# Kernel tuning notes

Hardware: AMD Instinct MI355X
Metric: run time of the kernel (lower is better)

The kernel has to match this reference:

```python
import jax, jax.numpy as jnp
import numpy as np

# Model constants (match init_kwargs / input_specs)
D_MODEL = 64; N_HEADS = 4; D_HEAD = D_MODEL // N_HEADS
N_LAYERS = 2; D_FF = 256
N_GRAPHS = 256; NODES_PER = 64; N_NODES = N_GRAPHS * NODES_PER
DEG = 8; N_EDGES = N_NODES * DEG
VOCAB = 32; N_CLASS = 10


def setup_inputs() -> dict:
    rng = np.random.default_rng(0)
    # node labels
    x = jnp.asarray(rng.integers(0, VOCAB, N_NODES), dtype=jnp.int32)
    # sparse edge_index: each node receives DEG messages from random nodes in its own graph
    base = np.repeat(np.arange(N_NODES), DEG)
    nbr = (base // NODES_PER) * NODES_PER + rng.integers(0, NODES_PER, N_NODES * DEG)
    edge_index = jnp.asarray(np.stack([nbr, base]), dtype=jnp.int32)  # [2, E] (src, dst)
    # complete_edge_index: all (src, dst) pairs within each graph
    local = np.arange(NODES_PER); goff = np.arange(N_GRAPHS) * NODES_PER
    ii = np.repeat(local, NODES_PER); jj = np.tile(local, NODES_PER)
    c_src = (goff[:, None] + ii[None, :]).reshape(-1)
    c_dst = (goff[:, None] + jj[None, :]).reshape(-1)
    complete_edge_index = jnp.asarray(np.stack([c_src, c_dst]), dtype=jnp.int32)  # [2, 1048576]
    batch = jnp.asarray(np.repeat(np.arange(N_GRAPHS), NODES_PER), dtype=jnp.int32)

    key = jax.random.key(0)
    ks = jax.random.split(key, 12)
    s = 1.0 / np.sqrt(D_MODEL)
    W = lambda k, shape, sc: jax.random.normal(k, shape, jnp.float32) * sc
    return {
        'x': x, 'edge_index': edge_index, 'complete_edge_index': complete_edge_index, 'batch': batch,
        'emb': W(ks[0], (VOCAB, D_MODEL), 0.1),
        'Wg_self': W(ks[1], (N_LAYERS, D_MODEL, D_MODEL), s),
        'Wg_nbr': W(ks[2], (N_LAYERS, D_MODEL, D_MODEL), s),
        'Wq': W(ks[3], (N_LAYERS, D_MODEL, D_MODEL), s),
        'Wk': W(ks[4], (N_LAYERS, D_MODEL, D_MODEL), s),
        'Wv': W(ks[5], (N_LAYERS, D_MODEL, D_MODEL), s),
        'Wo': W(ks[6], (N_LAYERS, D_MODEL, D_MODEL), s),
        'bo': jnp.zeros((N_LAYERS, D_MODEL), jnp.float32),
        'ln1_g': jnp.ones((N_LAYERS, D_MODEL), jnp.float32),
        'ln1_b': jnp.zeros((N_LAYERS, D_MODEL), jnp.float32),
        'ff_W1': W(ks[7], (N_LAYERS, D_MODEL, D_FF), s),
        'ff_b1': jnp.zeros((N_LAYERS, D_FF), jnp.float32),
        'ff_W2': W(ks[8], (N_LAYERS, D_FF, D_MODEL), 1.0 / np.sqrt(D_FF)),
        'ff_b2': jnp.zeros((N_LAYERS, D_MODEL), jnp.float32),
        'ln2_g': jnp.ones((N_LAYERS, D_MODEL), jnp.float32),
        'ln2_b': jnp.zeros((N_LAYERS, D_MODEL), jnp.float32),
        'c_W1': W(ks[9], (D_MODEL, D_MODEL), s),
        'c_b1': jnp.zeros((D_MODEL,), jnp.float32),
        'c_W2': W(ks[10], (D_MODEL, N_CLASS), s),
        'c_b2': jnp.zeros((N_CLASS,), jnp.float32),
    }


def _layernorm(h, g, b):
    m = jnp.mean(h, -1, keepdims=True)
    v = jnp.var(h, -1, keepdims=True)
    return (h - m) * jax.lax.rsqrt(v + 1e-5) * g + b


def _forward(x, edge_index, complete_edge_index, batch, emb, Wg_self, Wg_nbr, Wq, Wk, Wv, Wo, bo,
             ln1_g, ln1_b, ff_W1, ff_b1, ff_W2, ff_b2, ln2_g, ln2_b, c_W1, c_b1, c_W2, c_b2):
    e_src, e_dst = edge_index[0], edge_index[1]
    c_src, c_dst = complete_edge_index[0], complete_edge_index[1]
    h = emb[x]  # [N, d] embedding lookup
    inv_sqrt = 1.0 / np.sqrt(D_HEAD)
    for i in range(N_LAYERS):
        # --- structure extractor: one GNN message-passing step over sparse edge_index ---
        agg = jax.ops.segment_sum((h @ Wg_nbr[i])[e_src], e_dst, num_segments=N_NODES)
        struct = h + jax.nn.relu(h @ Wg_self[i] + agg)
        # --- multi-head attention over complete_edge_index (full attention within graph) ---
        q = (struct @ Wq[i]).reshape(N_NODES, N_HEADS, D_HEAD)
        k = (struct @ Wk[i]).reshape(N_NODES, N_HEADS, D_HEAD)
        v = (h @ Wv[i]).reshape(N_NODES, N_HEADS, D_HEAD)
        scores = jnp.einsum('ehd,ehd->eh', q[c_dst], k[c_src]) * inv_sqrt  # [Ec, H]
        m = jax.ops.segment_max(scores, c_dst, num_segments=N_NODES)
        ex = jnp.exp(scores - m[c_dst])
        den = jax.ops.segment_sum(ex, c_dst, num_segments=N_NODES)
        alpha = ex / den[c_dst]  # segment softmax per destination node
        attn = jax.ops.segment_sum(alpha[:, :, None] * v[c_src], c_dst, num_segments=N_NODES)
        out = attn.reshape(N_NODES, D_MODEL) @ Wo[i] + bo[i]
        h = _layernorm(h + out, ln1_g[i], ln1_b[i])
        # --- feed-forward ---
        f = jax.nn.relu(h @ ff_W1[i] + ff_b1[i]) @ ff_W2[i] + ff_b2[i]
        h = _layernorm(h + f, ln2_g[i], ln2_b[i])
    # --- global mean pooling per graph + classifier ---
    counts = jax.ops.segment_sum(jnp.ones((N_NODES,), jnp.float32), batch, num_segments=N_GRAPHS)
    pooled = jax.ops.segment_sum(h, batch, num_segments=N_GRAPHS) / counts[:, None]
    return jax.nn.relu(pooled @ c_W1 + c_b1) @ c_W2 + c_b2  # [B, num_class]


def reference(x, edge_index, complete_edge_index, batch, emb, Wg_self, Wg_nbr, Wq, Wk, Wv, Wo, bo,
              ln1_g, ln1_b, ff_W1, ff_b1, ff_W2, ff_b2, ln2_g, ln2_b, c_W1, c_b1, c_W2, c_b2):
    return _forward(x, edge_index, complete_edge_index, batch, emb, Wg_self, Wg_nbr, Wq, Wk, Wv, Wo,
                    bo, ln1_g, ln1_b, ff_W1, ff_b1, ff_W2, ff_b2, ln2_g, ln2_b, c_W1, c_b1, c_W2, c_b2)
```

## Files before the change

### kernel.cpp

```cpp
#include <hip/hip_runtime.h>

#define NG 256
#define NPG 64
#define DM 64
#define DFF 256
#define NL 2
#define DEG 8
#define NCLS 10
#define S68 68
#define S132 132

#define HB0 0
#define AB0 4352
#define BB0 8704
#define QB0 13056
#define F10 17408
#define POOLW 25856

#define FF1B 98304
#define FF2B 163840
#define WTOT 229376

__device__ __align__(16) unsigned short g_w[WTOT];

typedef __attribute__((ext_vector_type(4))) float f32x4;
typedef __attribute__((ext_vector_type(4))) unsigned int u32x4;
typedef __attribute__((ext_vector_type(8))) __bf16 bf16x8;

__device__ __forceinline__ unsigned int packsplit(float x) {
    union { float f; unsigned int u; } a; a.f = x;
    const unsigned int t = a.u;
    const unsigned int hi = (t + 0x7FFFu + ((t >> 16) & 1u)) >> 16;
    union { unsigned int u; float f; } hf; hf.u = hi << 16;
    union { float f; unsigned int u; } b; b.f = x - hf.f;
    const unsigned int tl = b.u;
    const unsigned int lo = (tl + 0x7FFFu + ((tl >> 16) & 1u)) & 0xFFFF0000u;
    return hi | lo;
}
__device__ __forceinline__ float unpackf(unsigned int u) {
    union { unsigned int u; float f; } h, l;
    h.u = u << 16;
    l.u = u & 0xFFFF0000u;
    return h.f + l.f;
}

__device__ __forceinline__ void extract(u32x4 p0, u32x4 p1, u32x4& hi, u32x4& lo) {
    hi[0] = (p0[0] & 0xFFFFu) | (p0[1] << 16);
    hi[1] = (p0[2] & 0xFFFFu) | (p0[3] << 16);
    hi[2] = (p1[0] & 0xFFFFu) | (p1[1] << 16);
    hi[3] = (p1[2] & 0xFFFFu) | (p1[3] << 16);
    lo[0] = (p0[0] >> 16) | (p0[1] & 0xFFFF0000u);
    lo[1] = (p0[2] >> 16) | (p0[3] & 0xFFFF0000u);
    lo[2] = (p1[0] >> 16) | (p1[1] & 0xFFFF0000u);
    lo[3] = (p1[2] >> 16) | (p1[3] & 0xFFFF0000u);
}

__device__ __forceinline__ bf16x8 ld8(const unsigned short* p) { return *(const bf16x8*)p; }

__device__ __forceinline__ f32x4 mfma16(u32x4 a, bf16x8 b, f32x4 c) {
    return __builtin_amdgcn_mfma_f32_16x16x32_bf16(__builtin_bit_cast(bf16x8, a), b, c, 0, 0, 0);
}

struct AP2 { u32x4 h, l; };
__device__ __forceinline__ AP2 loadA32(const unsigned int* p) {
    const u32x4 a0 = *(const u32x4*)p, a1 = *(const u32x4*)(p + 4);
    AP2 r; extract(a0, a1, r.h, r.l); return r;
}

__device__ __forceinline__ f32x4 chunkp(const AP2& a, const unsigned short* bhp, int plane,
                                        f32x4 acc) {
    const bf16x8 bh = ld8(bhp), bl = ld8(bhp + plane);
    acc = mfma16(a.h, bh, acc);
    acc = mfma16(a.h, bl, acc);
    acc = mfma16(a.l, bh, acc);
    return acc;
}

__device__ __forceinline__ f32x4 mm64p(const AP2& a0, const AP2& a1,
                                       const unsigned short* Wh, int boff) {
    f32x4 acc = {0.f, 0.f, 0.f, 0.f};
    acc = chunkp(a0, Wh + boff,      4096, acc);
    acc = chunkp(a1, Wh + boff + 32, 4096, acc);
    return acc;
}

__device__ __forceinline__ void dwrite_f32(float* dst, f32x4 acc, int wr, int wc, int l) {
    const int col = (wc << 4) + (l & 15);
    const int r0 = (wr << 4) + ((l >> 4) << 2);
#pragma unroll
    for (int r = 0; r < 4; ++r) dst[(r0 + r) * S68 + col] = acc[r];
}

__device__ __forceinline__ void layernorm(const float* src, unsigned int* dst,
                                          const float* gp, const float* bp, int n, int jg) {
    const f32x4 v = *(const f32x4*)(src + n * S68 + jg);
    float s1 = v[0] + v[1] + v[2] + v[3];
    float s2 = v[0]*v[0] + v[1]*v[1] + v[2]*v[2] + v[3]*v[3];
    s1 += __shfl_xor(s1, 1); s1 += __shfl_xor(s1, 2);
    s1 += __shfl_xor(s1, 4); s1 += __shfl_xor(s1, 8);
    s2 += __shfl_xor(s2, 1); s2 += __shfl_xor(s2, 2);
    s2 += __shfl_xor(s2, 4); s2 += __shfl_xor(s2, 8);
    const float mean = s1 * 0.015625f;
    const float var  = s2 * 0.015625f - mean * mean;
    const float rstd = rsqrtf(var + 1e-5f);
    const f32x4 gm = *(const f32x4*)(gp + jg);
    const f32x4 bt = *(const f32x4*)(bp + jg);
    u32x4 p;
#pragma unroll
    for (int j = 0; j < 4; ++j) p[j] = packsplit((v[j] - mean) * rstd * gm[j] + bt[j]);
    *(u32x4*)(dst + n * S68 + jg) = p;
}

extern "C" __global__ void gt_prep(const float* __restrict__ Wgn, const float* __restrict__ Wgs,
                                   const float* __restrict__ Wk, const float* __restrict__ Wq,
                                   const float* __restrict__ Wv, const float* __restrict__ Wo,
                                   const float* __restrict__ fW1, const float* __restrict__ fW2,
                                   unsigned short* wout)
{
    unsigned short* W = wout ? wout : g_w;
    const int t = blockIdx.x * 256 + threadIdx.x;
    float v; int dhi, plane;
    if (t < 49152) {
        const int m = t >> 12, r = t & 4095, k = r >> 6, c = r & 63;
        const int lay = m / 6, idx = m - lay * 6;
        const float* s;
        switch (idx) { case 0: s = Wgn; break; case 1: s = Wgs; break;
                       case 2: s = Wk;  break; case 3: s = Wq;  break;
                       case 4: s = Wv;  break; default: s = Wo; }
        v = s[lay * 4096 + k * 64 + c];
        dhi = (m << 13) + (c << 6) + k;
        plane = 4096;
    } else if (t < 81920) {
        const int r = t - 49152, lay = r >> 14, q = r & 16383, k = q >> 8, c = q & 255;
        v = fW1[lay * 16384 + k * 256 + c];
        dhi = FF1B + lay * 32768 + (c << 6) + k;
        plane = 16384;
    } else {
        const int r = t - 81920, lay = r >> 14, q = r & 16383, k = q >> 6, c = q & 63;
        v = fW2[lay * 16384 + k * 64 + c];
        dhi = FF2B + lay * 32768 + (c << 8) + k;
        plane = 16384;
    }
    union { float f; unsigned int u; } a; a.f = v;
    const unsigned int hi = (a.u + 0x7FFFu + ((a.u >> 16) & 1u)) >> 16;
    union { unsigned int u; float f; } hf; hf.u = hi << 16;
    union { float f; unsigned int u; } b; b.f = v - hf.f;
    const unsigned int lo = (b.u + 0x7FFFu + ((b.u >> 16) & 1u)) >> 16;
    W[dhi] = (unsigned short)hi;
    W[dhi + plane] = (unsigned short)lo;
}

extern "C" __global__ __launch_bounds__(1024)
void gt_main(const int* __restrict__ x, const int* __restrict__ e_src,
             const float* __restrict__ emb, const float* __restrict__ bo,
             const float* __restrict__ l1g, const float* __restrict__ l1b,
             const float* __restrict__ fb1, const float* __restrict__ fb2,
             const float* __restrict__ l2g, const float* __restrict__ l2b,
             const float* __restrict__ cW1, const float* __restrict__ cb1,
             const float* __restrict__ cW2, const float* __restrict__ cb2,
             const unsigned short* __restrict__ wext,
             float* __restrict__ out)
{
    const unsigned short* gww = wext ? wext : g_w;

    __shared__ __align__(16) unsigned int pool[POOLW];
    unsigned int* Hb  = pool + HB0;
    unsigned int* Abu = pool + AB0;  float* Abf = (float*)Abu;
    float* Bbf = (float*)(pool + BB0);
    float* Qbf = (float*)(pool + QB0);
    float* Vbf = (float*)(pool + F10);
    unsigned int* F1  = pool + F10;

    const int g = blockIdx.x, tid = threadIdx.x;
    const int w = tid >> 6, l = tid & 63;
    const int wr = w >> 2, wc = w & 3;
    const int n = tid >> 4, jg = (tid & 15) << 2;

    const int arow = (wr << 4) + (l & 15);
    const int bcol = (wc << 4) + (l & 15);
    const int kg   = (l >> 4) << 3;
    const int boff = (bcol << 6) + kg;

    {
        const int lbl = x[g * NPG + n];
        const f32x4 e = *(const f32x4*)(emb + lbl * DM + jg);
        u32x4 p;
#pragma unroll
        for (int j = 0; j < 4; ++j) p[j] = packsplit(e[j]);
        *(u32x4*)(Hb + n * S68 + jg) = p;
    }
    __syncthreads();

    for (int lay = 0; lay < NL; ++lay) {
        const unsigned short* Wm = gww + ((lay * 6) << 13);

        {
            const unsigned int* Ar = Hb + arow * S68;
            const AP2 a0 = loadA32(Ar + kg), a1 = loadA32(Ar + kg + 32);
            dwrite_f32(Abf, mm64p(a0, a1, Wm,               boff), wr, wc, l);
            dwrite_f32(Qbf, mm64p(a0, a1, Wm + (1 << 13),   boff), wr, wc, l);
            dwrite_f32(Vbf, mm64p(a0, a1, Wm + (4 << 13),   boff), wr, wc, l);
        }
        __syncthreads();

        {
            f32x4 s = {0.f, 0.f, 0.f, 0.f};
            const int* es = e_src + (g * NPG + n) * DEG;
#pragma unroll
            for (int k = 0; k < DEG; ++k) {
                const int sr = es[k] - g * NPG;
                const f32x4 v4 = *(const f32x4*)(Abf + sr * S68 + jg);
                s[0] += v4[0]; s[1] += v4[1]; s[2] += v4[2]; s[3] += v4[3];
            }
            *(f32x4*)(Bbf + n * S68 + jg) = s;
        }
        __syncthreads();

        {
            const f32x4 u4 = *(const f32x4*)(Qbf + n * S68 + jg);
            const f32x4 a4 = *(const f32x4*)(Bbf + n * S68 + jg);
            const u32x4 hp = *(const u32x4*)(Hb + n * S68 + jg);
            u32x4 p;
#pragma unroll
            for (int j = 0; j < 4; ++j)
                p[j] = packsplit(unpackf(hp[j]) + fmaxf(u4[j] + a4[j], 0.f));
            *(u32x4*)(Abu + n * S68 + jg) = p;
        }
        __syncthreads();

        {
            const unsigned int* Ar = Abu + arow * S68;
            const AP2 a0 = loadA32(Ar + kg), a1 = loadA32(Ar + kg + 32);
            dwrite_f32(Bbf, mm64p(a0, a1, Wm + (2 << 13), boff), wr, wc, l);
            dwrite_f32(Qbf, mm64p(a0, a1, Wm + (3 << 13), boff), wr, wc, l);
        }
        __syncthreads();

        {
            const f32x4 qr = *(const f32x4*)(Qbf + n * S68 + jg);
            const float q0 = qr[0] * 0.25f, q1 = qr[1] * 0.25f;
            const float q2 = qr[2] * 0.25f, q3 = qr[3] * 0.25f;
            float o0 = 0.f, o1 = 0.f, o2 = 0.f, o3 = 0.f, m = -1e30f, ls = 0.f;
#pragma unroll 4
            for (int sr = 0; sr < NPG; ++sr) {
                const f32x4 k4 = *(const f32x4*)(Bbf + sr * S68 + jg);
                float s = q0*k4[0] + q1*k4[1] + q2*k4[2] + q3*k4[3];
                s += __shfl_xor(s, 1);
                s += __shfl_xor(s, 2);
                const float mn  = fmaxf(m, s);
                const float fac = __expf(m - mn), wg = __expf(s - mn);
                ls = ls * fac + wg;
                const f32x4 v4 = *(const f32x4*)(Vbf + sr * S68 + jg);
                o0 = o0 * fac + wg * v4[0]; o1 = o1 * fac + wg * v4[1];
                o2 = o2 * fac + wg * v4[2]; o3 = o3 * fac + wg * v4[3];
                m = mn;
            }
            const float il = 1.f / ls;
            u32x4 p;
            p[0] = packsplit(o0 * il); p[1] = packsplit(o1 * il);
            p[2] = packsplit(o2 * il); p[3] = packsplit(o3 * il);
            *(u32x4*)(Abu + n * S68 + jg) = p;
        }
        __syncthreads();

        {
            const unsigned int* Ar = Abu + arow * S68;
            const AP2 a0 = loadA32(Ar + kg), a1 = loadA32(Ar + kg + 32);
            const f32x4 acc = mm64p(a0, a1, Wm + (5 << 13), boff);
            const int r0 = (wr << 4) + ((l >> 4) << 2);
            const float bb = bo[lay * DM + bcol];
#pragma unroll
            for (int r = 0; r < 4; ++r) {
                const int row = r0 + r;
                Bbf[row * S68 + bcol] = acc[r] + bb + unpackf(Hb[row * S68 + bcol]);
            }
        }
        __syncthreads();

        layernorm(Bbf, Hb, l1g + lay * DM, l1b + lay * DM, n, jg);
        __syncthreads();

        f32x4 f2 = {0.f, 0.f, 0.f, 0.f};
        for (int hf = 0; hf < 2; ++hf) {
            {
                const unsigned int* Ar = Hb + arow * S68;
                const AP2 a0 = loadA32(Ar + kg), a1 = loadA32(Ar + kg + 32);
                const unsigned short* B1 = gww + FF1B + lay * 32768;
                const int r0 = (wr << 4) + ((l >> 4) << 2);
#pragma unroll
                for (int t = 0; t < 2; ++t) {
                    const int tc = ((wc + 4 * t) << 4) + (l & 15);
                    const int cg = hf * 128 + tc;
                    f32x4 acc = {0.f, 0.f, 0.f, 0.f};
                    acc = chunkp(a0, B1 + (cg << 6) + kg,      16384, acc);
                    acc = chunkp(a1, B1 + (cg << 6) + kg + 32, 16384, acc);
                    const float b1 = fb1[lay * DFF + cg];
#pragma unroll
                    for (int r = 0; r < 4; ++r)
                        F1[(r0 + r) * S132 + tc] = packsplit(fmaxf(acc[r] + b1, 0.f));
                }
            }
            __syncthreads();
            {
                const unsigned int* Ar = F1 + arow * S132;
                const unsigned short* B2 = gww + FF2B + lay * 32768 + (bcol << 8) + hf * 128;
#pragma unroll
                for (int ch = 0; ch < 4; ++ch) {
                    const AP2 ac = loadA32(Ar + kg + 32 * ch);
                    f2 = chunkp(ac, B2 + kg + 32 * ch, 16384, f2);
                }
            }
            __syncthreads();
        }
        {
            const int r0 = (wr << 4) + ((l >> 4) << 2);
            const float bb = fb2[lay * DM + bcol];
#pragma unroll
            for (int r = 0; r < 4; ++r) {
                const int row = r0 + r;
                Abf[row * S68 + bcol] = f2[r] + bb + unpackf(Hb[row * S68 + bcol]);
            }
        }
        __syncthreads();

        layernorm(Abf, Hb, l2g + lay * DM, l2b + lay * DM, n, jg);
        __syncthreads();
    }

    if (tid < DM) {
        float s = 0.f;
        for (int nn = 0; nn < NPG; ++nn) s += unpackf(Hb[nn * S68 + tid]);
        Abf[tid] = s * 0.015625f;
    }
    __syncthreads();
    if (tid < DM) {
        float acc = cb1[tid];
        for (int i = 0; i < DM; ++i) acc = fmaf(Abf[i], cW1[i * DM + tid], acc);
        Bbf[tid] = fmaxf(acc, 0.f);
    }
    __syncthreads();
    if (tid < NCLS) {
        float acc = cb2[tid];
        for (int i = 0; i < DM; ++i) acc = fmaf(Bbf[i], cW2[i * NCLS + tid], acc);
        out[g * NCLS + tid] = acc;
    }
}

extern "C" void kernel_launch(void* const* d_in, const int* in_sizes, int n_in,
                              void* d_out, int out_size, void* d_ws, size_t ws_size,
                              hipStream_t stream) {
    unsigned short* wbuf =
        (d_ws != nullptr && ws_size >= (size_t)WTOT * 2) ? (unsigned short*)d_ws : nullptr;
    gt_prep<<<dim3(448), dim3(256), 0, stream>>>(
        (const float*)d_in[6], (const float*)d_in[5],
        (const float*)d_in[8], (const float*)d_in[7],
        (const float*)d_in[9], (const float*)d_in[10],
        (const float*)d_in[14], (const float*)d_in[16],
        wbuf);
    gt_main<<<dim3(NG), dim3(1024), 0, stream>>>(
        (const int*)d_in[0], (const int*)d_in[1],
        (const float*)d_in[4], (const float*)d_in[11],
        (const float*)d_in[12], (const float*)d_in[13],
        (const float*)d_in[15], (const float*)d_in[17],
        (const float*)d_in[18], (const float*)d_in[19],
        (const float*)d_in[20], (const float*)d_in[21],
        (const float*)d_in[22], (const float*)d_in[23],
        wbuf,
        (float*)d_out);
}
```

Baseline: 96.26 us.

## Stage 64x64 weights in swizzled LDS with prefetch overlapping compute phases

Weights are now stored as interleaved hi/lo bf16 pairs in one 32-bit word rather than two separate planes. The six 64x64 projection matrices per layer are staged into three XOR-swizzled LDS buffers. Each buffer is refilled from global memory during an earlier phase so the load overlaps other work, and the MFMA B operands are then read from LDS instead of global memory. This raises LDS use to about 150KB per block, which still fits at one block per CU. It also adds register pressure from prefetched values held across phases, plus extract work on the B operands.

```diff
diff --git a/kernel.cpp b/kernel.cpp
--- a/kernel.cpp
+++ b/kernel.cpp
@@ -15,13 +15,14 @@
 #define BB0 8704
 #define QB0 13056
 #define F10 17408
-#define POOLW 25856
-
-#define FF1B 98304
-#define FF2B 163840
-#define WTOT 229376
-
-__device__ __align__(16) unsigned short g_w[WTOT];
+#define WSB 25856
+#define POOLW 38144
+
+#define FF1B 49152
+#define FF2B 81920
+#define WTOT 114688
+
+__device__ __align__(16) unsigned int g_w[WTOT];
 
 typedef __attribute__((ext_vector_type(4))) float f32x4;
 typedef __attribute__((ext_vector_type(4))) unsigned int u32x4;
@@ -55,10 +56,9 @@
     lo[3] = (p1[2] >> 16) | (p1[3] & 0xFFFF0000u);
 }
 
-__device__ __forceinline__ bf16x8 ld8(const unsigned short* p) { return *(const bf16x8*)p; }
-
-__device__ __forceinline__ f32x4 mfma16(u32x4 a, bf16x8 b, f32x4 c) {
-    return __builtin_amdgcn_mfma_f32_16x16x32_bf16(__builtin_bit_cast(bf16x8, a), b, c, 0, 0, 0);
+__device__ __forceinline__ f32x4 mfma16(u32x4 a, u32x4 b, f32x4 c) {
+    return __builtin_amdgcn_mfma_f32_16x16x32_bf16(
+        __builtin_bit_cast(bf16x8, a), __builtin_bit_cast(bf16x8, b), c, 0, 0, 0);
 }
 
 struct AP2 { u32x4 h, l; };
@@ -67,20 +67,28 @@
     AP2 r; extract(a0, a1, r.h, r.l); return r;
 }
 
-__device__ __forceinline__ f32x4 chunkp(const AP2& a, const unsigned short* bhp, int plane,
-                                        f32x4 acc) {
-    const bf16x8 bh = ld8(bhp), bl = ld8(bhp + plane);
+__device__ __forceinline__ f32x4 chunkAB(const AP2& a, u32x4 w0, u32x4 w1, f32x4 acc) {
+    u32x4 bh, bl;
+    extract(w0, w1, bh, bl);
     acc = mfma16(a.h, bh, acc);
     acc = mfma16(a.h, bl, acc);
     acc = mfma16(a.l, bh, acc);
     return acc;
 }
-
-__device__ __forceinline__ f32x4 mm64p(const AP2& a0, const AP2& a1,
-                                       const unsigned short* Wh, int boff) {
+__device__ __forceinline__ f32x4 chunkG(const AP2& a, const unsigned int* p, f32x4 acc) {
+    return chunkAB(a, *(const u32x4*)p, *(const u32x4*)(p + 4), acc);
+}
+
+__device__ __forceinline__ f32x4 mmS(const AP2& a0, const AP2& a1,
+                                     const unsigned int* Wb, int bcol, int kg) {
+    const int rb = bcol << 6, cx = bcol & 7, q0 = kg >> 2;
+    const u32x4 w00 = *(const u32x4*)(Wb + rb + (((q0    ) ^ cx) << 2));
+    const u32x4 w01 = *(const u32x4*)(Wb + rb + (((q0 + 1) ^ cx) << 2));
+    const u32x4 w10 = *(const u32x4*)(Wb + rb + (((q0 + 8) ^ cx) << 2));
+    const u32x4 w11 = *(const u32x4*)(Wb + rb + (((q0 + 9) ^ cx) << 2));
     f32x4 acc = {0.f, 0.f, 0.f, 0.f};
-    acc = chunkp(a0, Wh + boff,      4096, acc);
-    acc = chunkp(a1, Wh + boff + 32, 4096, acc);
+    acc = chunkAB(a0, w00, w01, acc);
+    acc = chunkAB(a1, w10, w11, acc);
     return acc;
 }
 
@@ -115,11 +123,11 @@
                                    const float* __restrict__ Wk, const float* __restrict__ Wq,
                                    const float* __restrict__ Wv, const float* __restrict__ Wo,
                                    const float* __restrict__ fW1, const float* __restrict__ fW2,
-                                   unsigned short* wout)
+                                   unsigned int* wout)
 {
-    unsigned short* W = wout ? wout : g_w;
+    unsigned int* W = wout ? wout : g_w;
     const int t = blockIdx.x * 256 + threadIdx.x;
-    float v; int dhi, plane;
+    float v; int d;
     if (t < 49152) {
         const int m = t >> 12, r = t & 4095, k = r >> 6, c = r & 63;
         const int lay = m / 6, idx = m - lay * 6;
@@ -128,26 +136,17 @@
                        case 2: s = Wk;  break; case 3: s = Wq;  break;
                        case 4: s = Wv;  break; default: s = Wo; }
         v = s[lay * 4096 + k * 64 + c];
-        dhi = (m << 13) + (c << 6) + k;
-        plane = 4096;
+        d = (m << 12) + (c << 6) + ((((k >> 2) ^ (c & 7)) << 2) | (k & 3));
     } else if (t < 81920) {
         const int r = t - 49152, lay = r >> 14, q = r & 16383, k = q >> 8, c = q & 255;
         v = fW1[lay * 16384 + k * 256 + c];
-        dhi = FF1B + lay * 32768 + (c << 6) + k;
-        plane = 16384;
+        d = FF1B + lay * 16384 + (c << 6) + k;
     } else {
         const int r = t - 81920, lay = r >> 14, q = r & 16383, k = q >> 6, c = q & 63;
         v = fW2[lay * 16384 + k * 64 + c];
-        dhi = FF2B + lay * 32768 + (c << 8) + k;
-        plane = 16384;
-    }
-    union { float f; unsigned int u; } a; a.f = v;
-    const unsigned int hi = (a.u + 0x7FFFu + ((a.u >> 16) & 1u)) >> 16;
-    union { unsigned int u; float f; } hf; hf.u = hi << 16;
-    union { float f; unsigned int u; } b; b.f = v - hf.f;
-    const unsigned int lo = (b.u + 0x7FFFu + ((b.u >> 16) & 1u)) >> 16;
-    W[dhi] = (unsigned short)hi;
-    W[dhi + plane] = (unsigned short)lo;
+        d = FF2B + lay * 16384 + (c << 8) + k;
+    }
+    W[d] = packsplit(v);
 }
 
 extern "C" __global__ __launch_bounds__(1024)
@@ -158,10 +157,10 @@
              const float* __restrict__ l2g, const float* __restrict__ l2b,
              const float* __restrict__ cW1, const float* __restrict__ cb1,
              const float* __restrict__ cW2, const float* __restrict__ cb2,
-             const unsigned short* __restrict__ wext,
+             const unsigned int* __restrict__ wext,
              float* __restrict__ out)
 {
-    const unsigned short* gww = wext ? wext : g_w;
+    const unsigned int* gw = wext ? wext : g_w;
 
     __shared__ __align__(16) unsigned int pool[POOLW];
     unsigned int* Hb  = pool + HB0;
@@ -170,6 +169,9 @@
     float* Qbf = (float*)(pool + QB0);
     float* Vbf = (float*)(pool + F10);
     unsigned int* F1  = pool + F10;
+    unsigned int* Wb0 = pool + WSB;
+    unsigned int* Wb1 = pool + WSB + 4096;
+    unsigned int* Wb2 = pool + WSB + 8192;
 
     const int g = blockIdx.x, tid = threadIdx.x;
     const int w = tid >> 6, l = tid & 63;
@@ -179,31 +181,39 @@
     const int arow = (wr << 4) + (l & 15);
     const int bcol = (wc << 4) + (l & 15);
     const int kg   = (l >> 4) << 3;
-    const int boff = (bcol << 6) + kg;
+    const int t4   = tid << 2;
 
     {
+        const u32x4 s0 = *(const u32x4*)(gw + (0 << 12) + t4);
+        const u32x4 s1 = *(const u32x4*)(gw + (1 << 12) + t4);
+        const u32x4 s2 = *(const u32x4*)(gw + (4 << 12) + t4);
         const int lbl = x[g * NPG + n];
         const f32x4 e = *(const f32x4*)(emb + lbl * DM + jg);
         u32x4 p;
 #pragma unroll
         for (int j = 0; j < 4; ++j) p[j] = packsplit(e[j]);
         *(u32x4*)(Hb + n * S68 + jg) = p;
+        *(u32x4*)(Wb0 + t4) = s0;
+        *(u32x4*)(Wb1 + t4) = s1;
+        *(u32x4*)(Wb2 + t4) = s2;
     }
     __syncthreads();
 
     for (int lay = 0; lay < NL; ++lay) {
-        const unsigned short* Wm = gww + ((lay * 6) << 13);
+        const bool pre = (lay + 1 < NL);
 
         {
             const unsigned int* Ar = Hb + arow * S68;
             const AP2 a0 = loadA32(Ar + kg), a1 = loadA32(Ar + kg + 32);
-            dwrite_f32(Abf, mm64p(a0, a1, Wm,               boff), wr, wc, l);
-            dwrite_f32(Qbf, mm64p(a0, a1, Wm + (1 << 13),   boff), wr, wc, l);
-            dwrite_f32(Vbf, mm64p(a0, a1, Wm + (4 << 13),   boff), wr, wc, l);
-        }
-        __syncthreads();
-
-        {
+            dwrite_f32(Abf, mmS(a0, a1, Wb0, bcol, kg), wr, wc, l);
+            dwrite_f32(Qbf, mmS(a0, a1, Wb1, bcol, kg), wr, wc, l);
+            dwrite_f32(Vbf, mmS(a0, a1, Wb2, bcol, kg), wr, wc, l);
+        }
+        __syncthreads();
+
+        {
+            const u32x4 t0 = *(const u32x4*)(gw + ((lay * 6 + 2) << 12) + t4);
+            const u32x4 t1 = *(const u32x4*)(gw + ((lay * 6 + 3) << 12) + t4);
             f32x4 s = {0.f, 0.f, 0.f, 0.f};
             const int* es = e_src + (g * NPG + n) * DEG;
 #pragma unroll
@@ -213,10 +223,13 @@
                 s[0] += v4[0]; s[1] += v4[1]; s[2] += v4[2]; s[3] += v4[3];
             }
             *(f32x4*)(Bbf + n * S68 + jg) = s;
-        }
-        __syncthreads();
-
-        {
+            *(u32x4*)(Wb0 + t4) = t0;
+            *(u32x4*)(Wb1 + t4) = t1;
+        }
+        __syncthreads();
+
+        {
+            const u32x4 t2 = *(const u32x4*)(gw + ((lay * 6 + 5) << 12) + t4);
             const f32x4 u4 = *(const f32x4*)(Qbf + n * S68 + jg);
             const f32x4 a4 = *(const f32x4*)(Bbf + n * S68 + jg);
             const u32x4 hp = *(const u32x4*)(Hb + n * S68 + jg);
@@ -225,18 +238,24 @@
             for (int j = 0; j < 4; ++j)
                 p[j] = packsplit(unpackf(hp[j]) + fmaxf(u4[j] + a4[j], 0.f));
             *(u32x4*)(Abu + n * S68 + jg) = p;
+            *(u32x4*)(Wb2 + t4) = t2;
         }
         __syncthreads();
 
         {
             const unsigned int* Ar = Abu + arow * S68;
             const AP2 a0 = loadA32(Ar + kg), a1 = loadA32(Ar + kg + 32);
-            dwrite_f32(Bbf, mm64p(a0, a1, Wm + (2 << 13), boff), wr, wc, l);
-            dwrite_f32(Qbf, mm64p(a0, a1, Wm + (3 << 13), boff), wr, wc, l);
-        }
-        __syncthreads();
-
-        {
+            dwrite_f32(Bbf, mmS(a0, a1, Wb0, bcol, kg), wr, wc, l);
+            dwrite_f32(Qbf, mmS(a0, a1, Wb1, bcol, kg), wr, wc, l);
+        }
+        __syncthreads();
+
+        {
+            u32x4 t0, t1;
+            if (pre) {
+                t0 = *(const u32x4*)(gw + (((lay + 1) * 6 + 0) << 12) + t4);
+                t1 = *(const u32x4*)(gw + (((lay + 1) * 6 + 1) << 12) + t4);
+            }
             const f32x4 qr = *(const f32x4*)(Qbf + n * S68 + jg);
             const float q0 = qr[0] * 0.25f, q1 = qr[1] * 0.25f;
             const float q2 = qr[2] * 0.25f, q3 = qr[3] * 0.25f;
@@ -260,13 +279,17 @@
             p[0] = packsplit(o0 * il); p[1] = packsplit(o1 * il);
             p[2] = packsplit(o2 * il); p[3] = packsplit(o3 * il);
             *(u32x4*)(Abu + n * S68 + jg) = p;
+            if (pre) {
+                *(u32x4*)(Wb0 + t4) = t0;
+                *(u32x4*)(Wb1 + t4) = t1;
+            }
         }
         __syncthreads();
 
         {
             const unsigned int* Ar = Abu + arow * S68;
             const AP2 a0 = loadA32(Ar + kg), a1 = loadA32(Ar + kg + 32);
-            const f32x4 acc = mm64p(a0, a1, Wm + (5 << 13), boff);
+            const f32x4 acc = mmS(a0, a1, Wb2, bcol, kg);
             const int r0 = (wr << 4) + ((l >> 4) << 2);
             const float bb = bo[lay * DM + bcol];
 #pragma unroll
@@ -277,7 +300,12 @@
         }
         __syncthreads();
 
-        layernorm(Bbf, Hb, l1g + lay * DM, l1b + lay * DM, n, jg);
+        {
+            u32x4 t2;
+            if (pre) t2 = *(const u32x4*)(gw + (((lay + 1) * 6 + 4) << 12) + t4);
+            layernorm(Bbf, Hb, l1g + lay * DM, l1b + lay * DM, n, jg);
+            if (pre) *(u32x4*)(Wb2 + t4) = t2;
+        }
         __syncthreads();
 
         f32x4 f2 = {0.f, 0.f, 0.f, 0.f};
@@ -285,15 +313,16 @@
             {
                 const unsigned int* Ar = Hb + arow * S68;
                 const AP2 a0 = loadA32(Ar + kg), a1 = loadA32(Ar + kg + 32);
-                const unsigned short* B1 = gww + FF1B + lay * 32768;
+                const unsigned int* B1 = gw + FF1B + lay * 16384;
                 const int r0 = (wr << 4) + ((l >> 4) << 2);
 #pragma unroll
                 for (int t = 0; t < 2; ++t) {
                     const int tc = ((wc + 4 * t) << 4) + (l & 15);
                     const int cg = hf * 128 + tc;
+                    const unsigned int* Bp = B1 + (cg << 6);
                     f32x4 acc = {0.f, 0.f, 0.f, 0.f};
-                    acc = chunkp(a0, B1 + (cg << 6) + kg,      16384, acc);
-                    acc = chunkp(a1, B1 + (cg << 6) + kg + 32, 16384, acc);
+                    acc = chunkG(a0, Bp + kg,      acc);
+                    acc = chunkG(a1, Bp + kg + 32, acc);
                     const float b1 = fb1[lay * DFF + cg];
 #pragma unroll
                     for (int r = 0; r < 4; ++r)
@@ -303,11 +332,11 @@
             __syncthreads();
             {
                 const unsigned int* Ar = F1 + arow * S132;
-                const unsigned short* B2 = gww + FF2B + lay * 32768 + (bcol << 8) + hf * 128;
+                const unsigned int* B2 = gw + FF2B + lay * 16384 + (bcol << 8) + hf * 128;
 #pragma unroll
                 for (int ch = 0; ch < 4; ++ch) {
                     const AP2 ac = loadA32(Ar + kg + 32 * ch);
-                    f2 = chunkp(ac, B2 + kg + 32 * ch, 16384, f2);
+                    f2 = chunkG(ac, B2 + kg + 32 * ch, f2);
                 }
             }
             __syncthreads();
@@ -349,8 +378,8 @@
 extern "C" void kernel_launch(void* const* d_in, const int* in_sizes, int n_in,
                               void* d_out, int out_size, void* d_ws, size_t ws_size,
                               hipStream_t stream) {
-    unsigned short* wbuf =
-        (d_ws != nullptr && ws_size >= (size_t)WTOT * 2) ? (unsigned short*)d_ws : nullptr;
+    unsigned int* wbuf =
+        (d_ws != nullptr && ws_size >= (size_t)WTOT * 4) ? (unsigned int*)d_ws : nullptr;
     gt_prep<<<dim3(448), dim3(256), 0, stream>>>(
         (const float*)d_in[6], (const float*)d_in[5],
         (const float*)d_in[8], (const float*)d_in[7],
```

After: 82.54 us. 14.2% less time.

## Stage 64x64 layer weights in XOR-swizzled LDS with prefetch across phases

Applied to the files above, without the earlier changes.

The six 64x64 per-layer weight matrices (hi/lo bf16 planes) are now copied into three shared-memory buffers, using an XOR swizzle on the k-groups so MFMA B-operand reads avoid bank conflicts. Loads for the next-needed matrices are issued during earlier compute phases and written to LDS before the following barrier, overlapping global fetch with work. The cost is about 48KB of extra LDS per block, which can only matter for occupancy if several blocks would otherwise fit per CU. The feed-forward weights still stream from global memory.

```diff
diff --git a/kernel.cpp b/kernel.cpp
--- a/kernel.cpp
+++ b/kernel.cpp
@@ -15,13 +15,14 @@
 #define BB0 8704
 #define QB0 13056
 #define F10 17408
-#define POOLW 25856
-
-#define FF1B 98304
-#define FF2B 163840
-#define WTOT 229376
-
-__device__ __align__(16) unsigned short g_w[WTOT];
+#define WSB 25856
+#define POOLW 38144
+
+#define FF1B16 98304
+#define FF2B16 163840
+#define WTOT16 229376
+
+__device__ __align__(16) unsigned short g_w[WTOT16];
 
 typedef __attribute__((ext_vector_type(4))) float f32x4;
 typedef __attribute__((ext_vector_type(4))) unsigned int u32x4;
@@ -67,20 +68,26 @@
     AP2 r; extract(a0, a1, r.h, r.l); return r;
 }
 
-__device__ __forceinline__ f32x4 chunkp(const AP2& a, const unsigned short* bhp, int plane,
-                                        f32x4 acc) {
-    const bf16x8 bh = ld8(bhp), bl = ld8(bhp + plane);
+__device__ __forceinline__ f32x4 chunkB(const AP2& a, bf16x8 bh, bf16x8 bl, f32x4 acc) {
     acc = mfma16(a.h, bh, acc);
     acc = mfma16(a.h, bl, acc);
     acc = mfma16(a.l, bh, acc);
     return acc;
 }
-
-__device__ __forceinline__ f32x4 mm64p(const AP2& a0, const AP2& a1,
-                                       const unsigned short* Wh, int boff) {
+__device__ __forceinline__ f32x4 chunkPl(const AP2& a, const unsigned short* bp, int plane,
+                                         f32x4 acc) {
+    return chunkB(a, ld8(bp), ld8(bp + plane), acc);
+}
+
+__device__ __forceinline__ f32x4 mmS(const AP2& a0, const AP2& a1,
+                                     const unsigned int* Wb, int bcol, int kg) {
+    const unsigned short* P = (const unsigned short*)Wb;
+    const int row = bcol << 6, cx = bcol & 7, u0 = kg >> 3;
+    const unsigned short* p0 = P + row + (((u0    ) ^ cx) << 3);
+    const unsigned short* p1 = P + row + (((u0 + 4) ^ cx) << 3);
     f32x4 acc = {0.f, 0.f, 0.f, 0.f};
-    acc = chunkp(a0, Wh + boff,      4096, acc);
-    acc = chunkp(a1, Wh + boff + 32, 4096, acc);
+    acc = chunkB(a0, ld8(p0), ld8(p0 + 4096), acc);
+    acc = chunkB(a1, ld8(p1), ld8(p1 + 4096), acc);
     return acc;
 }
 
@@ -128,17 +135,17 @@
                        case 2: s = Wk;  break; case 3: s = Wq;  break;
                        case 4: s = Wv;  break; default: s = Wo; }
         v = s[lay * 4096 + k * 64 + c];
-        dhi = (m << 13) + (c << 6) + k;
+        dhi = (m << 13) + (c << 6) + ((((k >> 3) ^ (c & 7)) << 3) | (k & 7));
         plane = 4096;
     } else if (t < 81920) {
         const int r = t - 49152, lay = r >> 14, q = r & 16383, k = q >> 8, c = q & 255;
         v = fW1[lay * 16384 + k * 256 + c];
-        dhi = FF1B + lay * 32768 + (c << 6) + k;
+        dhi = FF1B16 + lay * 32768 + (c << 6) + k;
         plane = 16384;
     } else {
         const int r = t - 81920, lay = r >> 14, q = r & 16383, k = q >> 6, c = q & 63;
         v = fW2[lay * 16384 + k * 64 + c];
-        dhi = FF2B + lay * 32768 + (c << 8) + k;
+        dhi = FF2B16 + lay * 32768 + (c << 8) + k;
         plane = 16384;
     }
     union { float f; unsigned int u; } a; a.f = v;
@@ -161,7 +168,8 @@
              const unsigned short* __restrict__ wext,
              float* __restrict__ out)
 {
-    const unsigned short* gww = wext ? wext : g_w;
+    const unsigned short* gw16 = wext ? wext : g_w;
+    const unsigned int*   gwu  = (const unsigned int*)gw16;
 
     __shared__ __align__(16) unsigned int pool[POOLW];
     unsigned int* Hb  = pool + HB0;
@@ -170,6 +178,9 @@
     float* Qbf = (float*)(pool + QB0);
     float* Vbf = (float*)(pool + F10);
     unsigned int* F1  = pool + F10;
+    unsigned int* Wb0 = pool + WSB;
+    unsigned int* Wb1 = pool + WSB + 4096;
+    unsigned int* Wb2 = pool + WSB + 8192;
 
     const int g = blockIdx.x, tid = threadIdx.x;
     const int w = tid >> 6, l = tid & 63;
@@ -179,31 +190,39 @@
     const int arow = (wr << 4) + (l & 15);
     const int bcol = (wc << 4) + (l & 15);
     const int kg   = (l >> 4) << 3;
-    const int boff = (bcol << 6) + kg;
+    const int t4   = tid << 2;
 
     {
+        const u32x4 s0 = *(const u32x4*)(gwu + (0 << 12) + t4);
+        const u32x4 s1 = *(const u32x4*)(gwu + (1 << 12) + t4);
+        const u32x4 s2 = *(const u32x4*)(gwu + (4 << 12) + t4);
         const int lbl = x[g * NPG + n];
         const f32x4 e = *(const f32x4*)(emb + lbl * DM + jg);
         u32x4 p;
 #pragma unroll
         for (int j = 0; j < 4; ++j) p[j] = packsplit(e[j]);
         *(u32x4*)(Hb + n * S68 + jg) = p;
+        *(u32x4*)(Wb0 + t4) = s0;
+        *(u32x4*)(Wb1 + t4) = s1;
+        *(u32x4*)(Wb2 + t4) = s2;
     }
     __syncthreads();
 
     for (int lay = 0; lay < NL; ++lay) {
-        const unsigned short* Wm = gww + ((lay * 6) << 13);
+        const bool pre = (lay + 1 < NL);
 
         {
             const unsigned int* Ar = Hb + arow * S68;
             const AP2 a0 = loadA32(Ar + kg), a1 = loadA32(Ar + kg + 32);
-            dwrite_f32(Abf, mm64p(a0, a1, Wm,               boff), wr, wc, l);
-            dwrite_f32(Qbf, mm64p(a0, a1, Wm + (1 << 13),   boff), wr, wc, l);
-            dwrite_f32(Vbf, mm64p(a0, a1, Wm + (4 << 13),   boff), wr, wc, l);
-        }
-        __syncthreads();
-
-        {
+            dwrite_f32(Abf, mmS(a0, a1, Wb0, bcol, kg), wr, wc, l);
+            dwrite_f32(Qbf, mmS(a0, a1, Wb1, bcol, kg), wr, wc, l);
+            dwrite_f32(Vbf, mmS(a0, a1, Wb2, bcol, kg), wr, wc, l);
+        }
+        __syncthreads();
+
+        {
+            const u32x4 t0 = *(const u32x4*)(gwu + ((lay * 6 + 2) << 12) + t4);
+            const u32x4 t1 = *(const u32x4*)(gwu + ((lay * 6 + 3) << 12) + t4);
             f32x4 s = {0.f, 0.f, 0.f, 0.f};
             const int* es = e_src + (g * NPG + n) * DEG;
 #pragma unroll
@@ -213,10 +232,13 @@
                 s[0] += v4[0]; s[1] += v4[1]; s[2] += v4[2]; s[3] += v4[3];
             }
             *(f32x4*)(Bbf + n * S68 + jg) = s;
-        }
-        __syncthreads();
-
-        {
+            *(u32x4*)(Wb0 + t4) = t0;
+            *(u32x4*)(Wb1 + t4) = t1;
+        }
+        __syncthreads();
+
+        {
+            const u32x4 t2 = *(const u32x4*)(gwu + ((lay * 6 + 5) << 12) + t4);
             const f32x4 u4 = *(const f32x4*)(Qbf + n * S68 + jg);
             const f32x4 a4 = *(const f32x4*)(Bbf + n * S68 + jg);
             const u32x4 hp = *(const u32x4*)(Hb + n * S68 + jg);
@@ -225,18 +247,24 @@
             for (int j = 0; j < 4; ++j)
                 p[j] = packsplit(unpackf(hp[j]) + fmaxf(u4[j] + a4[j], 0.f));
             *(u32x4*)(Abu + n * S68 + jg) = p;
+            *(u32x4*)(Wb2 + t4) = t2;
         }
         __syncthreads();
 
         {
             const unsigned int* Ar = Abu + arow * S68;
             const AP2 a0 = loadA32(Ar + kg), a1 = loadA32(Ar + kg + 32);
-            dwrite_f32(Bbf, mm64p(a0, a1, Wm + (2 << 13), boff), wr, wc, l);
-            dwrite_f32(Qbf, mm64p(a0, a1, Wm + (3 << 13), boff), wr, wc, l);
-        }
-        __syncthreads();
-
-        {
+            dwrite_f32(Bbf, mmS(a0, a1, Wb0, bcol, kg), wr, wc, l);
+            dwrite_f32(Qbf, mmS(a0, a1, Wb1, bcol, kg), wr, wc, l);
+        }
+        __syncthreads();
+
+        {
+            u32x4 t0, t1;
+            if (pre) {
+                t0 = *(const u32x4*)(gwu + (((lay + 1) * 6 + 0) << 12) + t4);
+                t1 = *(const u32x4*)(gwu + (((lay + 1) * 6 + 1) << 12) + t4);
+            }
             const f32x4 qr = *(const f32x4*)(Qbf + n * S68 + jg);
             const float q0 = qr[0] * 0.25f, q1 = qr[1] * 0.25f;
             const float q2 = qr[2] * 0.25f, q3 = qr[3] * 0.25f;
@@ -260,13 +288,17 @@
             p[0] = packsplit(o0 * il); p[1] = packsplit(o1 * il);
             p[2] = packsplit(o2 * il); p[3] = packsplit(o3 * il);
             *(u32x4*)(Abu + n * S68 + jg) = p;
+            if (pre) {
+                *(u32x4*)(Wb0 + t4) = t0;
+                *(u32x4*)(Wb1 + t4) = t1;
+            }
         }
         __syncthreads();
 
         {
             const unsigned int* Ar = Abu + arow * S68;
             const AP2 a0 = loadA32(Ar + kg), a1 = loadA32(Ar + kg + 32);
-            const f32x4 acc = mm64p(a0, a1, Wm + (5 << 13), boff);
+            const f32x4 acc = mmS(a0, a1, Wb2, bcol, kg);
             const int r0 = (wr << 4) + ((l >> 4) << 2);
             const float bb = bo[lay * DM + bcol];
 #pragma unroll
@@ -277,7 +309,12 @@
         }
         __syncthreads();
 
-        layernorm(Bbf, Hb, l1g + lay * DM, l1b + lay * DM, n, jg);
+        {
+            u32x4 t2;
+            if (pre) t2 = *(const u32x4*)(gwu + (((lay + 1) * 6 + 4) << 12) + t4);
+            layernorm(Bbf, Hb, l1g + lay * DM, l1b + lay * DM, n, jg);
+            if (pre) *(u32x4*)(Wb2 + t4) = t2;
+        }
         __syncthreads();
 
         f32x4 f2 = {0.f, 0.f, 0.f, 0.f};
@@ -285,15 +322,16 @@
             {
                 const unsigned int* Ar = Hb + arow * S68;
                 const AP2 a0 = loadA32(Ar + kg), a1 = loadA32(Ar + kg + 32);
-                const unsigned short* B1 = gww + FF1B + lay * 32768;
+                const unsigned short* B1 = gw16 + FF1B16 + lay * 32768;
                 const int r0 = (wr << 4) + ((l >> 4) << 2);
 #pragma unroll
                 for (int t = 0; t < 2; ++t) {
                     const int tc = ((wc + 4 * t) << 4) + (l & 15);
                     const int cg = hf * 128 + tc;
+                    const unsigned short* Bp = B1 + (cg << 6);
                     f32x4 acc = {0.f, 0.f, 0.f, 0.f};
-                    acc = chunkp(a0, B1 + (cg << 6) + kg,      16384, acc);
-                    acc = chunkp(a1, B1 + (cg << 6) + kg + 32, 16384, acc);
+                    acc = chunkPl(a0, Bp + kg,      16384, acc);
+                    acc = chunkPl(a1, Bp + kg + 32, 16384, acc);
                     const float b1 = fb1[lay * DFF + cg];
 #pragma unroll
                     for (int r = 0; r < 4; ++r)
@@ -303,11 +341,11 @@
             __syncthreads();
             {
                 const unsigned int* Ar = F1 + arow * S132;
-                const unsigned short* B2 = gww + FF2B + lay * 32768 + (bcol << 8) + hf * 128;
+                const unsigned short* B2 = gw16 + FF2B16 + lay * 32768 + (bcol << 8) + hf * 128;
 #pragma unroll
                 for (int ch = 0; ch < 4; ++ch) {
                     const AP2 ac = loadA32(Ar + kg + 32 * ch);
-                    f2 = chunkp(ac, B2 + kg + 32 * ch, 16384, f2);
+                    f2 = chunkPl(ac, B2 + kg + 32 * ch, 16384, f2);
                 }
             }
             __syncthreads();
@@ -350,7 +388,7 @@
                               void* d_out, int out_size, void* d_ws, size_t ws_size,
                               hipStream_t stream) {
     unsigned short* wbuf =
-        (d_ws != nullptr && ws_size >= (size_t)WTOT * 2) ? (unsigned short*)d_ws : nullptr;
+        (d_ws != nullptr && ws_size >= (size_t)WTOT16 * 2) ? (unsigned short*)d_ws : nullptr;
     gt_prep<<<dim3(448), dim3(256), 0, stream>>>(
         (const float*)d_in[6], (const float*)d_in[5],
         (const float*)d_in[8], (const float*)d_in[7],
```

Result: faster. 80.46 us (-16.4%).
